# Kernel optimization log

Measured on AMD Instinct MI355X. Metric: run time of the kernel, lower is better.

The kernel has to match this reference:

```python
import jax, jax.numpy as jnp
import numpy as np

MARGIN = 0.1   # init kwarg m
EPS = 1e-6     # CosineSimilarity eps
B, D, C = 8192, 1024, 14
LABEL_P = 0.1


def setup_inputs() -> dict:
    key = jax.random.key(0)
    k1, k2 = jax.random.split(key)
    pred = jax.random.normal(k1, (B, D), dtype=jnp.float32)
    gt = (jax.random.uniform(k2, (B, C)) < LABEL_P).astype(jnp.float32)
    return {"pred": pred, "gt": gt}


def _cos(x, y):
    # torch.nn.CosineSimilarity(dim=1, eps=1e-6): dot / max(||x||*||y||, eps)
    dot = jnp.sum(x * y, axis=1)
    nx = jnp.sqrt(jnp.sum(x * x, axis=1))
    ny = jnp.sqrt(jnp.sum(y * y, axis=1))
    return dot / jnp.maximum(nx * ny, EPS)


def reference(pred, gt):
    n = pred.shape[0]
    has = jnp.sum(gt, axis=1) > 0                      # [B] labeled rows (idxs_a)
    share = (gt @ gt.T) > 0                            # [B,B] rows sharing any label
    # Labeled anchor: positives = rows sharing a label (incl. self),
    #                 negatives = setdiff(idxs_a, rows_pos) U idxs_n == ~share row.
    # Unlabeled anchor: positives = unlabeled rows, negatives = labeled rows.
    pos_mask = jnp.where(has[:, None], share, ~has[None, :])
    neg_mask = jnp.where(has[:, None], ~share, has[None, :])
    # Uniform sampling among masked columns via Gumbel-max (replaces random.sample)
    kp, kn = jax.random.split(jax.random.key(42))
    NEG_INF = jnp.float32(-1e30)
    pos_idx = jnp.argmax(jnp.where(pos_mask, jax.random.gumbel(kp, (n, n)), NEG_INF), axis=1)
    neg_idx = jnp.argmax(jnp.where(neg_mask, jax.random.gumbel(kn, (n, n)), NEG_INF), axis=1)
    anchor = pred
    positive = pred[pos_idx]
    negative = pred[neg_idx]
    cos_v = _cos(anchor, positive) - _cos(anchor, negative) + MARGIN
    return jnp.mean(jnp.maximum(cos_v, 0.0))
```

## Files before the change

### kernel.cpp

```cpp
#include <hip/hip_runtime.h>
#include <hip/hip_bf16.h>
#include <stdint.h>

#define NB 8192
#define ND 1024
#define NC 14

#define ROTL(x, r) __builtin_amdgcn_alignbit((x), (x), 32u - (r))
#define ADD3_IMM(x, s, imm) \
  asm("v_add3_u32 %0, %1, %2, " #imm : "=v"(x) : "v"(x), "v"(s))

static inline uint32_t rotl32h(uint32_t x, int r) { return (x << r) | (x >> (32 - r)); }
static void tf2x32_host(uint32_t k0, uint32_t k1, uint32_t x0, uint32_t x1,
                        uint32_t* o0, uint32_t* o1) {
  uint32_t ks[3] = { k0, k1, k0 ^ k1 ^ 0x1BD11BDAu };
  static const int R[8] = {13, 15, 26, 6, 17, 29, 16, 24};
  x0 += k0; x1 += k1;
  for (int g = 0; g < 5; ++g) {
    const int* rr = (g & 1) ? (R + 4) : R;
    for (int i = 0; i < 4; ++i) { x0 += x1; x1 = rotl32h(x1, rr[i]); x1 ^= x0; }
    x0 += ks[(g + 1) % 3];
    x1 += ks[(g + 2) % 3] + (uint32_t)(g + 1);
  }
  *o0 = x0; *o1 = x1;
}

__global__ void k_labels(const float* __restrict__ gt, uint32_t* __restrict__ lbits2) {
  const int i = blockIdx.x * 256 + threadIdx.x;
  uint32_t m = 0u;
#pragma unroll
  for (int c = 0; c < NC; ++c)
    m |= (gt[i * NC + c] != 0.0f) ? (1u << c) : 0u;
  lbits2[i] = m ? m : 0x4000u;
}

__global__ void __launch_bounds__(256) k_fused(
    const uint32_t* __restrict__ lbits2, const float* __restrict__ pred,
    uint32_t kp0, uint32_t kp1, uint32_t kps2,
    uint32_t kn0, uint32_t kn1, uint32_t kns2,
    float* __restrict__ losses) {
  const uint32_t tid = threadIdx.x;
  const int i = blockIdx.x;
  const uint32_t bi = lbits2[i];
  const uint32_t ftP = kp1 + ((uint32_t)i << 13) + tid;
  const uint32_t ftN = kn1 + ((uint32_t)i << 13) + tid;

  uint32_t bkP = 0u, bkN = 0u;

#pragma unroll 8
  for (uint32_t k = 0; k < 32; ++k) {
    const uint32_t bj = lbits2[tid + (k << 8)];
    const uint32_t m = bi & bj;
    const uint32_t s0 = m ? kp0 : kn0;
    const uint32_t s1 = m ? kp1 : kn1;
    const uint32_t s2 = m ? kps2 : kns2;
    uint32_t x0 = s0;
    uint32_t x1 = (m ? ftP : ftN) + (k << 8);
#define TFR(r) { x0 += x1; x1 = ROTL(x1, r); x1 ^= x0; }
    TFR(13) TFR(15) TFR(26) TFR(6)
    x0 += s1;  ADD3_IMM(x1, s2, 1);
    TFR(17) TFR(29) TFR(16) TFR(24)
    x0 += s2;  ADD3_IMM(x1, s0, 2);
    TFR(13) TFR(15) TFR(26) TFR(6)
    x0 += s0;  ADD3_IMM(x1, s1, 3);
    TFR(17) TFR(29) TFR(16) TFR(24)
    x0 += s1;  ADD3_IMM(x1, s2, 4);
    TFR(13) TFR(15) TFR(26) TFR(6)
    x0 += s2;  ADD3_IMM(x1, s0, 5);
#undef TFR
    const uint32_t t = x0 ^ x1;
    const uint32_t cand = ((t >> 9) << 5) + (31u - k);
    const uint32_t selP = m ? cand : 0u;
    const uint32_t selN = cand ^ selP;
    bkP = bkP > selP ? bkP : selP;
    bkN = bkN > selN ? bkN : selN;
  }

  uint32_t keyP = bkP >> 5, jP = tid + ((31u - (bkP & 31u)) << 8);
  uint32_t keyN = bkN >> 5, jN = tid + ((31u - (bkN & 31u)) << 8);
#pragma unroll
  for (int off = 32; off > 0; off >>= 1) {
    uint32_t k2 = __shfl_down(keyP, off, 64), j2 = __shfl_down(jP, off, 64);
    if (k2 > keyP || (k2 == keyP && j2 < jP)) { keyP = k2; jP = j2; }
    k2 = __shfl_down(keyN, off, 64); j2 = __shfl_down(jN, off, 64);
    if (k2 > keyN || (k2 == keyN && j2 < jN)) { keyN = k2; jN = j2; }
  }
  __shared__ uint32_t sk[2][4], sj[2][4];
  __shared__ int spn[2];
  const int wave = (int)tid >> 6, lane = (int)tid & 63;
  if (lane == 0) { sk[0][wave] = keyP; sj[0][wave] = jP; sk[1][wave] = keyN; sj[1][wave] = jN; }
  __syncthreads();
  if (tid == 0) {
    uint32_t bk = sk[0][0], bj = sj[0][0];
#pragma unroll
    for (int w = 1; w < 4; ++w)
      if (sk[0][w] > bk || (sk[0][w] == bk && sj[0][w] < bj)) { bk = sk[0][w]; bj = sj[0][w]; }
    spn[0] = (int)bj;
    bk = sk[1][0]; bj = sj[1][0];
#pragma unroll
    for (int w = 1; w < 4; ++w)
      if (sk[1][w] > bk || (sk[1][w] == bk && sj[1][w] < bj)) { bk = sk[1][w]; bj = sj[1][w]; }
    spn[1] = (int)bj;
  }
  __syncthreads();

  const int p = spn[0], n = spn[1];
  const float4* A  = (const float4*)(pred + (size_t)i * ND);
  const float4* P  = (const float4*)(pred + (size_t)p * ND);
  const float4* Nv = (const float4*)(pred + (size_t)n * ND);
  float4 a = A[tid], pv = P[tid], nv = Nv[tid];
  float na = a.x * a.x + a.y * a.y + a.z * a.z + a.w * a.w;
  float np = pv.x * pv.x + pv.y * pv.y + pv.z * pv.z + pv.w * pv.w;
  float nn = nv.x * nv.x + nv.y * nv.y + nv.z * nv.z + nv.w * nv.w;
  float dp = a.x * pv.x + a.y * pv.y + a.z * pv.z + a.w * pv.w;
  float dn = a.x * nv.x + a.y * nv.y + a.z * nv.z + a.w * nv.w;
#pragma unroll
  for (int o = 32; o > 0; o >>= 1) {
    na += __shfl_down(na, o, 64);
    np += __shfl_down(np, o, 64);
    nn += __shfl_down(nn, o, 64);
    dp += __shfl_down(dp, o, 64);
    dn += __shfl_down(dn, o, 64);
  }
  __shared__ float red[4][5];
  if (lane == 0) { red[wave][0] = na; red[wave][1] = np; red[wave][2] = nn;
                   red[wave][3] = dp; red[wave][4] = dn; }
  __syncthreads();
  if (tid == 0) {
    float NA = red[0][0] + red[1][0] + red[2][0] + red[3][0];
    float NP = red[0][1] + red[1][1] + red[2][1] + red[3][1];
    float NN = red[0][2] + red[1][2] + red[2][2] + red[3][2];
    float DP = red[0][3] + red[1][3] + red[2][3] + red[3][3];
    float DN = red[0][4] + red[1][4] + red[2][4] + red[3][4];
    NA = sqrtf(NA); NP = sqrtf(NP); NN = sqrtf(NN);
    float cp = DP / fmaxf(NA * NP, 1e-6f);
    float cn = DN / fmaxf(NA * NN, 1e-6f);
    losses[i] = fmaxf(cp - cn + 0.1f, 0.0f);
  }
}

__global__ void k_mean(const float* __restrict__ losses, float* __restrict__ out) {
  float s = 0.0f;
  for (int k = threadIdx.x; k < NB; k += 256) s += losses[k];
#pragma unroll
  for (int o = 32; o > 0; o >>= 1) s += __shfl_down(s, o, 64);
  __shared__ float red[4];
  int wave = threadIdx.x >> 6, lane = threadIdx.x & 63;
  if (lane == 0) red[wave] = s;
  __syncthreads();
  if (threadIdx.x == 0) out[0] = (red[0] + red[1] + red[2] + red[3]) / (float)NB;
}

extern "C" void kernel_launch(void* const* d_in, const int* in_sizes, int n_in,
                              void* d_out, int out_size, void* d_ws, size_t ws_size,
                              hipStream_t stream) {
  const float* pred = (const float*)d_in[0];
  const float* gt   = (const float*)d_in[1];
  float* out = (float*)d_out;

  char* ws = (char*)d_ws;
  uint32_t* lbits  = (uint32_t*)(ws);
  float*    losses = (float*)(ws + 32768);

  uint32_t kp0, kp1, kn0, kn1;
  tf2x32_host(0u, 42u, 0u, 0u, &kp0, &kp1);
  tf2x32_host(0u, 42u, 0u, 1u, &kn0, &kn1);
  const uint32_t kps2 = kp0 ^ kp1 ^ 0x1BD11BDAu;
  const uint32_t kns2 = kn0 ^ kn1 ^ 0x1BD11BDAu;

  k_labels<<<NB / 256, 256, 0, stream>>>(gt, lbits);
  k_fused<<<NB, 256, 0, stream>>>(lbits, pred, kp0, kp1, kps2, kn0, kn1, kns2, losses);
  k_mean<<<1, 256, 0, stream>>>(losses, out);
}
```

Measured before the change: 229.1 us.

## Fuse three kernels into one persistent cooperative kernel with grid syncs

Replaces the label, fused-row and mean kernels with a single cooperative persistent kernel that loops blocks over rows and uses grid-wide syncs between the phases. The aim is to remove two kernel launches and their inter-kernel gaps. The cost is grid.sync overhead, fewer resident blocks that must loop over rows, and an extra __syncthreads per row. The old three-kernel path remains as a fallback if the cooperative launch fails.

```diff
diff --git a/kernel.cpp b/kernel.cpp
--- a/kernel.cpp
+++ b/kernel.cpp
@@ -1,6 +1,9 @@
 #include <hip/hip_runtime.h>
 #include <hip/hip_bf16.h>
+#include <hip/hip_cooperative_groups.h>
 #include <stdint.h>
+
+namespace cg = cooperative_groups;
 
 #define NB 8192
 #define ND 1024
@@ -25,22 +28,12 @@
   *o0 = x0; *o1 = x1;
 }
 
-__global__ void k_labels(const float* __restrict__ gt, uint32_t* __restrict__ lbits2) {
-  const int i = blockIdx.x * 256 + threadIdx.x;
-  uint32_t m = 0u;
-#pragma unroll
-  for (int c = 0; c < NC; ++c)
-    m |= (gt[i * NC + c] != 0.0f) ? (1u << c) : 0u;
-  lbits2[i] = m ? m : 0x4000u;
-}
-
-__global__ void __launch_bounds__(256) k_fused(
-    const uint32_t* __restrict__ lbits2, const float* __restrict__ pred,
+__device__ __forceinline__ void do_row(
+    int i, uint32_t tid, const uint32_t* __restrict__ lbits2,
+    const float* __restrict__ pred,
     uint32_t kp0, uint32_t kp1, uint32_t kps2,
     uint32_t kn0, uint32_t kn1, uint32_t kns2,
     float* __restrict__ losses) {
-  const uint32_t tid = threadIdx.x;
-  const int i = blockIdx.x;
   const uint32_t bi = lbits2[i];
   const uint32_t ftP = kp1 + ((uint32_t)i << 13) + tid;
   const uint32_t ftN = kn1 + ((uint32_t)i << 13) + tid;
@@ -137,6 +130,61 @@
     float cn = DN / fmaxf(NA * NN, 1e-6f);
     losses[i] = fmaxf(cp - cn + 0.1f, 0.0f);
   }
+  __syncthreads();
+}
+
+__global__ void __launch_bounds__(256) k_all(
+    const float* __restrict__ gt, const float* __restrict__ pred,
+    uint32_t* __restrict__ lbits2, float* __restrict__ losses,
+    uint32_t kp0, uint32_t kp1, uint32_t kps2,
+    uint32_t kn0, uint32_t kn1, uint32_t kns2,
+    float* __restrict__ out) {
+  cg::grid_group grid = cg::this_grid();
+  const uint32_t tid = threadIdx.x;
+  const int b = blockIdx.x;
+  const int gsz = (int)gridDim.x;
+
+  for (int t = b * 256 + (int)tid; t < NB; t += gsz * 256) {
+    uint32_t m = 0u;
+#pragma unroll
+    for (int c = 0; c < NC; ++c)
+      m |= (gt[(size_t)t * NC + c] != 0.0f) ? (1u << c) : 0u;
+    lbits2[t] = m ? m : 0x4000u;
+  }
+  grid.sync();
+
+  for (int i = b; i < NB; i += gsz)
+    do_row(i, tid, lbits2, pred, kp0, kp1, kps2, kn0, kn1, kns2, losses);
+  grid.sync();
+
+  if (b == 0) {
+    float s = 0.0f;
+    for (int k = (int)tid; k < NB; k += 256) s += losses[k];
+#pragma unroll
+    for (int o = 32; o > 0; o >>= 1) s += __shfl_down(s, o, 64);
+    __shared__ float red2[4];
+    const int wave = (int)tid >> 6, lane = (int)tid & 63;
+    if (lane == 0) red2[wave] = s;
+    __syncthreads();
+    if (tid == 0) out[0] = (red2[0] + red2[1] + red2[2] + red2[3]) / (float)NB;
+  }
+}
+
+__global__ void k_labels(const float* __restrict__ gt, uint32_t* __restrict__ lbits2) {
+  const int i = blockIdx.x * 256 + threadIdx.x;
+  uint32_t m = 0u;
+#pragma unroll
+  for (int c = 0; c < NC; ++c)
+    m |= (gt[(size_t)i * NC + c] != 0.0f) ? (1u << c) : 0u;
+  lbits2[i] = m ? m : 0x4000u;
+}
+
+__global__ void __launch_bounds__(256) k_fused(
+    const uint32_t* __restrict__ lbits2, const float* __restrict__ pred,
+    uint32_t kp0, uint32_t kp1, uint32_t kps2,
+    uint32_t kn0, uint32_t kn1, uint32_t kns2,
+    float* __restrict__ losses) {
+  do_row(blockIdx.x, threadIdx.x, lbits2, pred, kp0, kp1, kps2, kn0, kn1, kns2, losses);
 }
 
 __global__ void k_mean(const float* __restrict__ losses, float* __restrict__ out) {
@@ -165,10 +213,24 @@
   uint32_t kp0, kp1, kn0, kn1;
   tf2x32_host(0u, 42u, 0u, 0u, &kp0, &kp1);
   tf2x32_host(0u, 42u, 0u, 1u, &kn0, &kn1);
-  const uint32_t kps2 = kp0 ^ kp1 ^ 0x1BD11BDAu;
-  const uint32_t kns2 = kn0 ^ kn1 ^ 0x1BD11BDAu;
-
-  k_labels<<<NB / 256, 256, 0, stream>>>(gt, lbits);
-  k_fused<<<NB, 256, 0, stream>>>(lbits, pred, kp0, kp1, kps2, kn0, kn1, kns2, losses);
-  k_mean<<<1, 256, 0, stream>>>(losses, out);
-}
+  uint32_t kps2 = kp0 ^ kp1 ^ 0x1BD11BDAu;
+  uint32_t kns2 = kn0 ^ kn1 ^ 0x1BD11BDAu;
+
+  int bpc = 0;
+  hipError_t qe = hipOccupancyMaxActiveBlocksPerMultiprocessor(&bpc, (const void*)k_all, 256, 0);
+  hipError_t le = hipErrorUnknown;
+  if (qe == hipSuccess && bpc > 0) {
+    int grid = bpc * 256;
+    if (grid > 2048) grid = 2048;
+    void* args[] = { (void*)&gt, (void*)&pred, (void*)&lbits, (void*)&losses,
+                     (void*)&kp0, (void*)&kp1, (void*)&kps2,
+                     (void*)&kn0, (void*)&kn1, (void*)&kns2, (void*)&out };
+    le = hipLaunchCooperativeKernel((const void*)k_all, dim3(grid), dim3(256),
+                                    args, 0, stream);
+  }
+  if (le != hipSuccess) {
+    k_labels<<<NB / 256, 256, 0, stream>>>(gt, lbits);
+    k_fused<<<NB, 256, 0, stream>>>(lbits, pred, kp0, kp1, kps2, kn0, kn1, kns2, losses);
+    k_mean<<<1, 256, 0, stream>>>(losses, out);
+  }
+}
```

Result: slower. 393.9 us (+71.9%).
